# Kernel optimization log

Hardware: AMD Instinct MI355X
Metric: run time of the kernel (lower is better)

Reference implementation:

```python
import jax, jax.numpy as jnp
import numpy as np

BATCH, T, IN, OUT, HID = 8, 4096, 128, 128, 256


def _glorot(key, shape, fan_in, fan_out):
    lim = np.sqrt(6.0 / (fan_in + fan_out))
    return jax.random.uniform(key, shape, jnp.float32, -lim, lim)


def setup_inputs() -> dict:
    key = jax.random.key(0)
    ks = jax.random.split(key, 9)
    # LRU init: r_min=0, r_max=1 => nu = -0.5*log(u), theta = pi/10 * u
    u1 = jax.random.uniform(ks[0], (HID,), jnp.float32, 1e-4, 1.0)
    nu_log = jnp.log(-0.5 * jnp.log(u1))
    theta = (jnp.pi / 10.0) * jax.random.uniform(ks[1], (HID,), jnp.float32, 1e-4, 1.0)
    theta_log = jnp.log(theta)
    return {
        "X": jax.random.normal(ks[2], (BATCH, T, IN), jnp.float32),
        "nu_log": nu_log,
        "theta_log": theta_log,
        "B_re": _glorot(ks[3], (HID, IN), IN, HID),
        "B_im": _glorot(ks[4], (HID, IN), IN, HID),
        "C_re": _glorot(ks[5], (OUT, HID), HID, OUT),
        "C_im": _glorot(ks[6], (OUT, HID), HID, OUT),
        "D": _glorot(ks[7], (OUT, IN), IN, OUT),
    }


def reference(X, nu_log, theta_log, B_re, B_im, C_re, C_im, D):
    # lambda = exp(-exp(nu_log) + 1j*exp(theta_log))  (diagonal complex decay)
    mag = jnp.exp(-jnp.exp(nu_log))            # [H]
    th = jnp.exp(theta_log)                    # [H]
    lam = (mag * jnp.cos(th) + 1j * (mag * jnp.sin(th))).astype(jnp.complex64)
    gamma = jnp.sqrt(1.0 - mag * mag)          # [H]
    Bc = (gamma[:, None] * (B_re + 1j * B_im)).astype(jnp.complex64)  # [H, IN]
    # Input projection: [B, T, H] complex
    BX = jnp.einsum('bti,hi->bth', X.astype(jnp.complex64), Bc)
    lam_b = jnp.broadcast_to(lam, BX.shape)

    def scan_fn(a, b):
        la, xa = a
        lb, xb = b
        return (la * lb, lb * xa + xb)

    _, hiddens = jax.lax.associative_scan(scan_fn, (lam_b, BX), axis=1)
    Cc = (C_re + 1j * C_im).astype(jnp.complex64)
    Y = jnp.real(jnp.einsum('bth,oh->bto', hiddens, Cc)) + jnp.einsum('bti,oi->bto', X, D)
    return Y
```

## Files before the change

kernel.cpp:

```cpp
#include <hip/hip_runtime.h>
#include <hip/hip_bf16.h>

#define TFULL 4096
#define NBATCH 8
#define INDIM 128
#define OUTDIM 128
#define HIDDIM 256
#define LCH 64
#define NCH (TFULL / LCH)

typedef float f32x4 __attribute__((ext_vector_type(4)));
typedef short short8 __attribute__((ext_vector_type(8)));

static __device__ __forceinline__ unsigned short f2bf(float f) {
    unsigned int x = __float_as_uint(f);
    x += 0x7fffu + ((x >> 16) & 1u);
    return (unsigned short)(x >> 16);
}
static __device__ __forceinline__ unsigned int pack2(float a, float b) {
    return ((unsigned int)f2bf(b) << 16) | (unsigned int)f2bf(a);
}
static __device__ __forceinline__ float bflo(unsigned int u) {
    return __uint_as_float(u << 16);
}
static __device__ __forceinline__ float bfhi(unsigned int u) {
    return __uint_as_float(u & 0xffff0000u);
}
static __device__ __forceinline__ void split2(float v, unsigned short& hi, unsigned short& lo) {
    hi = f2bf(v);
    lo = f2bf(v - __uint_as_float((unsigned int)hi << 16));
}

__global__ __launch_bounds__(256) void k_prep(
    const float* __restrict__ nu_log, const float* __restrict__ theta_log,
    const float* __restrict__ C_re, const float* __restrict__ C_im,
    const float* __restrict__ D,
    unsigned short* __restrict__ Wy_hi, unsigned short* __restrict__ Wy_lo,
    float2* __restrict__ lampow)
{
    int f = blockIdx.x * 256 + threadIdx.x;
    if (f < 81920) {
        int q = f;
        int kk = q & 63, o = (q >> 6) & 127, kc = q >> 13;
        int k = 64 * kc + kk;
        float v;
        if (k < 512) {
            int h = k >> 1;
            v = (k & 1) ? -C_im[o * HIDDIM + h] : C_re[o * HIDDIM + h];
        } else {
            v = D[o * INDIM + (k - 512)];
        }
        unsigned short hi, lo; split2(v, hi, lo);
        Wy_hi[q] = hi; Wy_lo[q] = lo;
    } else {
        int l = f - 81920;
        int h = l & 255, tl = l >> 8;
        float nu = expf(nu_log[h]), th = expf(theta_log[h]);
        float kf = (float)(tl + 1);
        float m = expf(-kf * nu);
        lampow[l] = make_float2(m * cosf(kf * th), m * sinf(kf * th));
    }
}

__global__ __launch_bounds__(256) void k_bx_scan(
    const float* __restrict__ X, const float* __restrict__ nu_log,
    const float* __restrict__ theta_log, const float* __restrict__ B_re,
    const float* __restrict__ B_im, unsigned int* __restrict__ hloc,
    float2* __restrict__ EC)
{
    __shared__ float smem[17024];
    float*  XT  = smem;
    float*  Brl = smem + 8704;
    float*  Bil = smem + 12864;
    float2* sb  = (float2*)smem;

    const int tid = threadIdx.x;
    const int blk = blockIdx.x;
    const int b   = blk >> 7;
    const int c   = (blk >> 1) & 63;
    const int h0  = (blk & 1) * 128;
    const int t0  = c * LCH;

    {
        const float* Xb = X + ((size_t)(b * TFULL + t0)) * INDIM;
        int r = tid >> 2;
        int q = tid & 3;
        #pragma unroll
        for (int k = 0; k < 8; ++k) {
            int slot = q + k * 4;
            float4 v = *(const float4*)(Xb + (size_t)r * INDIM + slot * 4);
            float* dst = XT + (slot * 4) * 68 + r;
            dst[0]      = v.x;
            dst[68]     = v.y;
            dst[2 * 68] = v.z;
            dst[3 * 68] = v.w;
        }
    }

    float accre[8][4], accim[8][4];
    #pragma unroll
    for (int r = 0; r < 8; ++r)
        #pragma unroll
        for (int j = 0; j < 4; ++j) { accre[r][j] = 0.f; accim[r][j] = 0.f; }

    const int ty = tid >> 5;
    const int tx = tid & 31;

    for (int kc = 0; kc < 4; ++kc) {
        __syncthreads();
        {
            int hr = tid >> 1;
            int s  = tid & 1;
            int hg = h0 + hr;
            float mag = expf(-expf(nu_log[hg]));
            float gam = sqrtf(fmaxf(0.f, 1.f - mag * mag));
            const float* br = B_re + (size_t)hg * INDIM + kc * 32;
            const float* bi = B_im + (size_t)hg * INDIM + kc * 32;
            #pragma unroll
            for (int q = 0; q < 4; ++q) {
                int col = s * 16 + q * 4;
                float4 vr = *(const float4*)(br + col);
                float4 vi = *(const float4*)(bi + col);
                Brl[(col + 0) * 130 + hr] = vr.x * gam;
                Brl[(col + 1) * 130 + hr] = vr.y * gam;
                Brl[(col + 2) * 130 + hr] = vr.z * gam;
                Brl[(col + 3) * 130 + hr] = vr.w * gam;
                Bil[(col + 0) * 130 + hr] = vi.x * gam;
                Bil[(col + 1) * 130 + hr] = vi.y * gam;
                Bil[(col + 2) * 130 + hr] = vi.z * gam;
                Bil[(col + 3) * 130 + hr] = vi.w * gam;
            }
        }
        __syncthreads();
        for (int kk = 0; kk < 32; ++kk) {
            const float* xrow = XT + (kc * 32 + kk) * 68 + ty * 8;
            float4 xa = *(const float4*)(xrow);
            float4 xb = *(const float4*)(xrow + 4);
            float2 br0 = *(const float2*)(Brl + kk * 130 + 2 * tx);
            float2 br1 = *(const float2*)(Brl + kk * 130 + 64 + 2 * tx);
            float2 bi0 = *(const float2*)(Bil + kk * 130 + 2 * tx);
            float2 bi1 = *(const float2*)(Bil + kk * 130 + 64 + 2 * tx);
            float xs[8]  = {xa.x, xa.y, xa.z, xa.w, xb.x, xb.y, xb.z, xb.w};
            float brs[4] = {br0.x, br0.y, br1.x, br1.y};
            float bis[4] = {bi0.x, bi0.y, bi1.x, bi1.y};
            #pragma unroll
            for (int r = 0; r < 8; ++r)
                #pragma unroll
                for (int j = 0; j < 4; ++j) {
                    accre[r][j] = fmaf(xs[r], brs[j], accre[r][j]);
                    accim[r][j] = fmaf(xs[r], bis[j], accim[r][j]);
                }
        }
    }

    __syncthreads();
    #pragma unroll
    for (int r = 0; r < 8; ++r) {
        int t = ty * 8 + r;
        #pragma unroll
        for (int j = 0; j < 4; ++j) {
            int hl = (j < 2) ? (2 * tx + j) : (64 + 2 * tx + (j - 2));
            sb[t * 130 + hl] = make_float2(accre[r][j], accim[r][j]);
        }
    }
    __syncthreads();

    if (tid < 128) {
        int hl = tid, hg = h0 + hl;
        float nu = expf(nu_log[hg]), th = expf(theta_log[hg]);
        float mag = expf(-nu);
        float lre = mag * cosf(th), lim = mag * sinf(th);
        float sre = 0.f, sim = 0.f;
        unsigned int* hout = hloc + (size_t)(b * TFULL + t0) * HIDDIM + h0 + hl;
        for (int t = 0; t < LCH; ++t) {
            float2 v = sb[t * 130 + hl];
            float nre = fmaf(lre, sre, fmaf(-lim, sim, v.x));
            float nim = fmaf(lre, sim, fmaf(lim, sre, v.y));
            sre = nre; sim = nim;
            hout[(size_t)t * HIDDIM] = pack2(sre, sim);
        }
        EC[((size_t)b * NCH + c) * HIDDIM + h0 + hl] = make_float2(sre, sim);
    }
}

__global__ __launch_bounds__(256) void k_carry(
    const float* __restrict__ nu_log, const float* __restrict__ theta_log,
    float2* __restrict__ EC)
{
    int b = blockIdx.x, h = threadIdx.x;
    float nu = expf(nu_log[h]), th = expf(theta_log[h]);
    float m = expf(-(float)LCH * nu);
    float Lre = m * cosf((float)LCH * th);
    float Lim = m * sinf((float)LCH * th);
    float cre = 0.f, cim = 0.f;
    for (int c = 0; c < NCH; ++c) {
        size_t idx = ((size_t)b * NCH + c) * HIDDIM + h;
        float2 e = EC[idx];
        EC[idx] = make_float2(cre, cim);
        float nre = e.x + Lre * cre - Lim * cim;
        float nim = e.y + Lre * cim + Lim * cre;
        cre = nre; cim = nim;
    }
}

__global__ __launch_bounds__(256) void k_y(
    const float* __restrict__ X, const unsigned int* __restrict__ hloc,
    const float2* __restrict__ EC, const float2* __restrict__ lampow,
    const unsigned short* __restrict__ Wy_hi,
    const unsigned short* __restrict__ Wy_lo, float* __restrict__ Y)
{
    __shared__ unsigned short sm[27648];
    unsigned short* Ah = sm;
    unsigned short* Al = sm + 4608;
    unsigned short* Bh = sm + 9216;
    unsigned short* Bl = sm + 18432;
    __shared__ float2 carryS[256];

    const int tid = threadIdx.x;
    const int b = blockIdx.x >> 6, c = blockIdx.x & 63;
    const size_t rowbase = (size_t)(b * TFULL + c * LCH);

    carryS[tid] = EC[((size_t)b * NCH + c) * HIDDIM + tid];

    f32x4 acc[2][4];
    #pragma unroll
    for (int mi = 0; mi < 2; ++mi)
        #pragma unroll
        for (int nj = 0; nj < 4; ++nj) acc[mi][nj] = (f32x4){0.f, 0.f, 0.f, 0.f};

    const int w = tid >> 6, l = tid & 63;
    const int wm = w >> 1, wn = w & 1;
    const int lr = l & 15, lk = l >> 4;

    for (int kc = 0; kc < 10; ++kc) {
        __syncthreads();
        {
            const uint4* sh = (const uint4*)(Wy_hi + kc * 8192);
            const uint4* sl = (const uint4*)(Wy_lo + kc * 8192);
            #pragma unroll
            for (int j = 0; j < 4; ++j) {
                uint4 vh = sh[tid + j * 256];
                uint4 vl = sl[tid + j * 256];
                int o = (tid >> 3) + 32 * j, kq = 8 * (tid & 7);
                *(uint4*)(Bh + o * 72 + kq) = vh;
                *(uint4*)(Bl + o * 72 + kq) = vl;
            }
        }
        if (kc < 8) {
            #pragma unroll
            for (int s = 0; s < 2; ++s) {
                int f = s * 256 + tid;
                int t = f >> 3, slot = f & 7;
                uint4 u = *(const uint4*)(hloc + (rowbase + t) * HIDDIM + 32 * kc + 4 * slot);
                unsigned int* Arh = (unsigned int*)Ah + t * 36 + 4 * slot;
                unsigned int* Arl = (unsigned int*)Al + t * 36 + 4 * slot;
                const unsigned int* uu = (const unsigned int*)&u;
                #pragma unroll
                for (int e = 0; e < 4; ++e) {
                    int h = 32 * kc + 4 * slot + e;
                    float2 lp = lampow[t * HIDDIM + h];
                    float2 cr = carryS[h];
                    float hre = bflo(uu[e]) + lp.x * cr.x - lp.y * cr.y;
                    float him = bfhi(uu[e]) + lp.x * cr.y + lp.y * cr.x;
                    unsigned short rh, rl, ih, il;
                    split2(hre, rh, rl); split2(him, ih, il);
                    Arh[e] = ((unsigned int)ih << 16) | rh;
                    Arl[e] = ((unsigned int)il << 16) | rl;
                }
            }
        } else {
            int i0 = (kc - 8) * 64;
            #pragma unroll
            for (int s = 0; s < 4; ++s) {
                int f = s * 256 + tid;
                int t = f >> 4, slot = f & 15;
                float4 v = *(const float4*)(X + (rowbase + t) * INDIM + i0 + 4 * slot);
                unsigned short h0,l0,h1,l1,h2,l2,h3,l3;
                split2(v.x,h0,l0); split2(v.y,h1,l1); split2(v.z,h2,l2); split2(v.w,h3,l3);
                unsigned int* Arh = (unsigned int*)Ah + t * 36 + 2 * slot;
                unsigned int* Arl = (unsigned int*)Al + t * 36 + 2 * slot;
                Arh[0] = ((unsigned int)h1 << 16) | h0;
                Arh[1] = ((unsigned int)h3 << 16) | h2;
                Arl[0] = ((unsigned int)l1 << 16) | l0;
                Arl[1] = ((unsigned int)l3 << 16) | l2;
            }
        }
        __syncthreads();
        #pragma unroll
        for (int ks = 0; ks < 2; ++ks) {
            short8 a0h = *(const short8*)(Ah + (32 * wm + lr) * 72 + 32 * ks + 8 * lk);
            short8 a1h = *(const short8*)(Ah + (32 * wm + 16 + lr) * 72 + 32 * ks + 8 * lk);
            short8 a0l = *(const short8*)(Al + (32 * wm + lr) * 72 + 32 * ks + 8 * lk);
            short8 a1l = *(const short8*)(Al + (32 * wm + 16 + lr) * 72 + 32 * ks + 8 * lk);
            #pragma unroll
            for (int nj = 0; nj < 4; ++nj) {
                short8 bh = *(const short8*)(Bh + (64 * wn + 16 * nj + lr) * 72 + 32 * ks + 8 * lk);
                short8 bl = *(const short8*)(Bl + (64 * wn + 16 * nj + lr) * 72 + 32 * ks + 8 * lk);
                acc[0][nj] = __builtin_amdgcn_mfma_f32_16x16x32_bf16(a0h, bh, acc[0][nj], 0, 0, 0);
                acc[0][nj] = __builtin_amdgcn_mfma_f32_16x16x32_bf16(a0h, bl, acc[0][nj], 0, 0, 0);
                acc[0][nj] = __builtin_amdgcn_mfma_f32_16x16x32_bf16(a0l, bh, acc[0][nj], 0, 0, 0);
                acc[1][nj] = __builtin_amdgcn_mfma_f32_16x16x32_bf16(a1h, bh, acc[1][nj], 0, 0, 0);
                acc[1][nj] = __builtin_amdgcn_mfma_f32_16x16x32_bf16(a1h, bl, acc[1][nj], 0, 0, 0);
                acc[1][nj] = __builtin_amdgcn_mfma_f32_16x16x32_bf16(a1l, bh, acc[1][nj], 0, 0, 0);
            }
        }
    }

    float* Yb = Y + rowbase * OUTDIM;
    #pragma unroll
    for (int mi = 0; mi < 2; ++mi)
        #pragma unroll
        for (int nj = 0; nj < 4; ++nj)
            #pragma unroll
            for (int r = 0; r < 4; ++r) {
                int t = 32 * wm + 16 * mi + 4 * lk + r;
                int o = 64 * wn + 16 * nj + lr;
                Yb[(size_t)t * OUTDIM + o] = acc[mi][nj][r];
            }
}

extern "C" void kernel_launch(void* const* d_in, const int* in_sizes, int n_in,
                              void* d_out, int out_size, void* d_ws, size_t ws_size,
                              hipStream_t stream) {
    const float* X         = (const float*)d_in[0];
    const float* nu_log    = (const float*)d_in[1];
    const float* theta_log = (const float*)d_in[2];
    const float* B_re      = (const float*)d_in[3];
    const float* B_im      = (const float*)d_in[4];
    const float* C_re      = (const float*)d_in[5];
    const float* C_im      = (const float*)d_in[6];
    const float* D         = (const float*)d_in[7];
    float* Y = (float*)d_out;

    unsigned int*   hloc   = (unsigned int*)d_ws;
    float2*         EC     = (float2*)((char*)d_ws + (size_t)33554432);
    float2*         lampow = (float2*)((char*)d_ws + (size_t)34603008);
    unsigned short* Wy_hi  = (unsigned short*)((char*)d_ws + (size_t)34996224);
    unsigned short* Wy_lo  = (unsigned short*)((char*)d_ws + (size_t)35160064);

    hipLaunchKernelGGL(k_prep, dim3(384), dim3(256), 0, stream,
                       nu_log, theta_log, C_re, C_im, D, Wy_hi, Wy_lo, lampow);
    hipLaunchKernelGGL(k_bx_scan, dim3(NBATCH * NCH * 2), dim3(256), 0, stream,
                       X, nu_log, theta_log, B_re, B_im, hloc, EC);
    hipLaunchKernelGGL(k_carry, dim3(NBATCH), dim3(256), 0, stream,
                       nu_log, theta_log, EC);
    hipLaunchKernelGGL(k_y, dim3(NBATCH * NCH), dim3(256), 0, stream,
                       X, hloc, EC, lampow, Wy_hi, Wy_lo, Y);
}
```

Before: 174.8 us.

## Move input projection to bf16x3 MFMA and split scan into separate kernel

The FP32 FMA input projection is replaced by a split-bf16 (hi/lo, three-product) MFMA GEMM. Gamma-scaled B weights are now pre-split once in the prep kernel. The per-chunk scan moves into its own kernel that works in place on an fp32 BX buffer. This uses matrix cores for the projection and lets all 256 threads run the scan instead of 128. In exchange, intermediate hidden states are now stored as fp32 complex rather than packed bf16, which doubles that workspace traffic, and there is one more kernel launch.

```diff
diff --git a/kernel.cpp b/kernel.cpp
--- a/kernel.cpp
+++ b/kernel.cpp
@@ -17,15 +17,6 @@
     x += 0x7fffu + ((x >> 16) & 1u);
     return (unsigned short)(x >> 16);
 }
-static __device__ __forceinline__ unsigned int pack2(float a, float b) {
-    return ((unsigned int)f2bf(b) << 16) | (unsigned int)f2bf(a);
-}
-static __device__ __forceinline__ float bflo(unsigned int u) {
-    return __uint_as_float(u << 16);
-}
-static __device__ __forceinline__ float bfhi(unsigned int u) {
-    return __uint_as_float(u & 0xffff0000u);
-}
 static __device__ __forceinline__ void split2(float v, unsigned short& hi, unsigned short& lo) {
     hi = f2bf(v);
     lo = f2bf(v - __uint_as_float((unsigned int)hi << 16));
@@ -33,14 +24,26 @@
 
 __global__ __launch_bounds__(256) void k_prep(
     const float* __restrict__ nu_log, const float* __restrict__ theta_log,
+    const float* __restrict__ B_re, const float* __restrict__ B_im,
     const float* __restrict__ C_re, const float* __restrict__ C_im,
     const float* __restrict__ D,
+    unsigned short* __restrict__ Wbx_hi, unsigned short* __restrict__ Wbx_lo,
     unsigned short* __restrict__ Wy_hi, unsigned short* __restrict__ Wy_lo,
     float2* __restrict__ lampow)
 {
     int f = blockIdx.x * 256 + threadIdx.x;
-    if (f < 81920) {
-        int q = f;
+    if (f < 65536) {
+        int kk = f & 31, n = (f >> 5) & 255, kc = (f >> 13) & 3, half = f >> 15;
+        int g = n >> 6;
+        int h = 128 * half + 64 * (g >> 1) + (n & 63);
+        int i = 32 * kc + kk;
+        float mag = expf(-expf(nu_log[h]));
+        float gam = sqrtf(fmaxf(0.f, 1.f - mag * mag));
+        float v = gam * ((g & 1) ? B_im[h * INDIM + i] : B_re[h * INDIM + i]);
+        unsigned short hi, lo; split2(v, hi, lo);
+        Wbx_hi[f] = hi; Wbx_lo[f] = lo;
+    } else if (f < 147456) {
+        int q = f - 65536;
         int kk = q & 63, o = (q >> 6) & 127, kc = q >> 13;
         int k = 64 * kc + kk;
         float v;
@@ -53,7 +56,7 @@
         unsigned short hi, lo; split2(v, hi, lo);
         Wy_hi[q] = hi; Wy_lo[q] = lo;
     } else {
-        int l = f - 81920;
+        int l = f - 147456;
         int h = l & 255, tl = l >> 8;
         float nu = expf(nu_log[h]), th = expf(theta_log[h]);
         float kf = (float)(tl + 1);
@@ -62,125 +65,118 @@
     }
 }
 
-__global__ __launch_bounds__(256) void k_bx_scan(
-    const float* __restrict__ X, const float* __restrict__ nu_log,
-    const float* __restrict__ theta_log, const float* __restrict__ B_re,
-    const float* __restrict__ B_im, unsigned int* __restrict__ hloc,
-    float2* __restrict__ EC)
-{
-    __shared__ float smem[17024];
-    float*  XT  = smem;
-    float*  Brl = smem + 8704;
-    float*  Bil = smem + 12864;
-    float2* sb  = (float2*)smem;
+__global__ __launch_bounds__(256) void k_bx(
+    const float* __restrict__ X,
+    const unsigned short* __restrict__ Wbx_hi,
+    const unsigned short* __restrict__ Wbx_lo,
+    float2* __restrict__ BX)
+{
+    __shared__ unsigned short sm[25600];
+    unsigned short* Ash = sm;
+    unsigned short* Asl = sm + 2560;
+    unsigned short* Bsh = sm + 5120;
+    unsigned short* Bsl = sm + 15360;
 
     const int tid = threadIdx.x;
     const int blk = blockIdx.x;
-    const int b   = blk >> 7;
-    const int c   = (blk >> 1) & 63;
-    const int h0  = (blk & 1) * 128;
-    const int t0  = c * LCH;
-
-    {
-        const float* Xb = X + ((size_t)(b * TFULL + t0)) * INDIM;
-        int r = tid >> 2;
-        int q = tid & 3;
-        #pragma unroll
-        for (int k = 0; k < 8; ++k) {
-            int slot = q + k * 4;
-            float4 v = *(const float4*)(Xb + (size_t)r * INDIM + slot * 4);
-            float* dst = XT + (slot * 4) * 68 + r;
-            dst[0]      = v.x;
-            dst[68]     = v.y;
-            dst[2 * 68] = v.z;
-            dst[3 * 68] = v.w;
-        }
-    }
-
-    float accre[8][4], accim[8][4];
+    const int b = blk >> 7, c = (blk >> 1) & 63, half = blk & 1;
+    const size_t rowbase = (size_t)(b * TFULL + c * LCH);
+
+    f32x4 acc[2][8];
     #pragma unroll
-    for (int r = 0; r < 8; ++r)
-        #pragma unroll
-        for (int j = 0; j < 4; ++j) { accre[r][j] = 0.f; accim[r][j] = 0.f; }
-
-    const int ty = tid >> 5;
-    const int tx = tid & 31;
+    for (int mi = 0; mi < 2; ++mi)
+        #pragma unroll
+        for (int j = 0; j < 8; ++j) acc[mi][j] = (f32x4){0.f, 0.f, 0.f, 0.f};
+
+    const int w = tid >> 6, l = tid & 63;
+    const int wm = w >> 1, wn = w & 1;
+    const int lr = l & 15, lk = l >> 4;
+    const unsigned short* wch_h = Wbx_hi + half * 32768;
+    const unsigned short* wch_l = Wbx_lo + half * 32768;
 
     for (int kc = 0; kc < 4; ++kc) {
         __syncthreads();
         {
-            int hr = tid >> 1;
-            int s  = tid & 1;
-            int hg = h0 + hr;
-            float mag = expf(-expf(nu_log[hg]));
-            float gam = sqrtf(fmaxf(0.f, 1.f - mag * mag));
-            const float* br = B_re + (size_t)hg * INDIM + kc * 32;
-            const float* bi = B_im + (size_t)hg * INDIM + kc * 32;
-            #pragma unroll
-            for (int q = 0; q < 4; ++q) {
-                int col = s * 16 + q * 4;
-                float4 vr = *(const float4*)(br + col);
-                float4 vi = *(const float4*)(bi + col);
-                Brl[(col + 0) * 130 + hr] = vr.x * gam;
-                Brl[(col + 1) * 130 + hr] = vr.y * gam;
-                Brl[(col + 2) * 130 + hr] = vr.z * gam;
-                Brl[(col + 3) * 130 + hr] = vr.w * gam;
-                Bil[(col + 0) * 130 + hr] = vi.x * gam;
-                Bil[(col + 1) * 130 + hr] = vi.y * gam;
-                Bil[(col + 2) * 130 + hr] = vi.z * gam;
-                Bil[(col + 3) * 130 + hr] = vi.w * gam;
+            const uint4* sh = (const uint4*)(wch_h + kc * 8192);
+            const uint4* sl = (const uint4*)(wch_l + kc * 8192);
+            #pragma unroll
+            for (int j = 0; j < 4; ++j) {
+                uint4 vh = sh[tid + j * 256];
+                uint4 vl = sl[tid + j * 256];
+                int n = (tid >> 2) + 64 * j, kq = 8 * (tid & 3);
+                *(uint4*)(Bsh + n * 40 + kq) = vh;
+                *(uint4*)(Bsl + n * 40 + kq) = vl;
+            }
+        }
+        {
+            int t = tid >> 2, q = tid & 3;
+            const float* Xr = X + (rowbase + t) * INDIM + 32 * kc + 8 * q;
+            float4 v0 = *(const float4*)(Xr);
+            float4 v1 = *(const float4*)(Xr + 4);
+            float xs[8] = {v0.x, v0.y, v0.z, v0.w, v1.x, v1.y, v1.z, v1.w};
+            unsigned int* Ah32 = (unsigned int*)Ash + t * 20 + 4 * q;
+            unsigned int* Al32 = (unsigned int*)Asl + t * 20 + 4 * q;
+            #pragma unroll
+            for (int e = 0; e < 4; ++e) {
+                unsigned short h0, l0, h1, l1;
+                split2(xs[2 * e], h0, l0);
+                split2(xs[2 * e + 1], h1, l1);
+                Ah32[e] = ((unsigned int)h1 << 16) | h0;
+                Al32[e] = ((unsigned int)l1 << 16) | l0;
             }
         }
         __syncthreads();
-        for (int kk = 0; kk < 32; ++kk) {
-            const float* xrow = XT + (kc * 32 + kk) * 68 + ty * 8;
-            float4 xa = *(const float4*)(xrow);
-            float4 xb = *(const float4*)(xrow + 4);
-            float2 br0 = *(const float2*)(Brl + kk * 130 + 2 * tx);
-            float2 br1 = *(const float2*)(Brl + kk * 130 + 64 + 2 * tx);
-            float2 bi0 = *(const float2*)(Bil + kk * 130 + 2 * tx);
-            float2 bi1 = *(const float2*)(Bil + kk * 130 + 64 + 2 * tx);
-            float xs[8]  = {xa.x, xa.y, xa.z, xa.w, xb.x, xb.y, xb.z, xb.w};
-            float brs[4] = {br0.x, br0.y, br1.x, br1.y};
-            float bis[4] = {bi0.x, bi0.y, bi1.x, bi1.y};
-            #pragma unroll
-            for (int r = 0; r < 8; ++r)
-                #pragma unroll
-                for (int j = 0; j < 4; ++j) {
-                    accre[r][j] = fmaf(xs[r], brs[j], accre[r][j]);
-                    accim[r][j] = fmaf(xs[r], bis[j], accim[r][j]);
-                }
-        }
-    }
-
-    __syncthreads();
+        short8 a0h = *(const short8*)(Ash + (32 * wm + lr) * 40 + 8 * lk);
+        short8 a1h = *(const short8*)(Ash + (32 * wm + 16 + lr) * 40 + 8 * lk);
+        short8 a0l = *(const short8*)(Asl + (32 * wm + lr) * 40 + 8 * lk);
+        short8 a1l = *(const short8*)(Asl + (32 * wm + 16 + lr) * 40 + 8 * lk);
+        #pragma unroll
+        for (int j = 0; j < 8; ++j) {
+            short8 bh = *(const short8*)(Bsh + (128 * wn + 16 * j + lr) * 40 + 8 * lk);
+            short8 bl = *(const short8*)(Bsl + (128 * wn + 16 * j + lr) * 40 + 8 * lk);
+            acc[0][j] = __builtin_amdgcn_mfma_f32_16x16x32_bf16(a0h, bh, acc[0][j], 0, 0, 0);
+            acc[0][j] = __builtin_amdgcn_mfma_f32_16x16x32_bf16(a0l, bh, acc[0][j], 0, 0, 0);
+            acc[0][j] = __builtin_amdgcn_mfma_f32_16x16x32_bf16(a0h, bl, acc[0][j], 0, 0, 0);
+            acc[1][j] = __builtin_amdgcn_mfma_f32_16x16x32_bf16(a1h, bh, acc[1][j], 0, 0, 0);
+            acc[1][j] = __builtin_amdgcn_mfma_f32_16x16x32_bf16(a1l, bh, acc[1][j], 0, 0, 0);
+            acc[1][j] = __builtin_amdgcn_mfma_f32_16x16x32_bf16(a1h, bl, acc[1][j], 0, 0, 0);
+        }
+    }
+
     #pragma unroll
-    for (int r = 0; r < 8; ++r) {
-        int t = ty * 8 + r;
-        #pragma unroll
-        for (int j = 0; j < 4; ++j) {
-            int hl = (j < 2) ? (2 * tx + j) : (64 + 2 * tx + (j - 2));
-            sb[t * 130 + hl] = make_float2(accre[r][j], accim[r][j]);
-        }
-    }
-    __syncthreads();
-
-    if (tid < 128) {
-        int hl = tid, hg = h0 + hl;
-        float nu = expf(nu_log[hg]), th = expf(theta_log[hg]);
-        float mag = expf(-nu);
-        float lre = mag * cosf(th), lim = mag * sinf(th);
-        float sre = 0.f, sim = 0.f;
-        unsigned int* hout = hloc + (size_t)(b * TFULL + t0) * HIDDIM + h0 + hl;
-        for (int t = 0; t < LCH; ++t) {
-            float2 v = sb[t * 130 + hl];
-            float nre = fmaf(lre, sre, fmaf(-lim, sim, v.x));
-            float nim = fmaf(lre, sim, fmaf(lim, sre, v.y));
-            sre = nre; sim = nim;
-            hout[(size_t)t * HIDDIM] = pack2(sre, sim);
-        }
-        EC[((size_t)b * NCH + c) * HIDDIM + h0 + hl] = make_float2(sre, sim);
-    }
+    for (int mi = 0; mi < 2; ++mi)
+        #pragma unroll
+        for (int j = 0; j < 4; ++j)
+            #pragma unroll
+            for (int r = 0; r < 4; ++r) {
+                int t = 32 * wm + 16 * mi + 4 * lk + r;
+                int h = 128 * half + 64 * wn + 16 * j + lr;
+                BX[(rowbase + t) * HIDDIM + h] =
+                    make_float2(acc[mi][j][r], acc[mi][j + 4][r]);
+            }
+}
+
+__global__ __launch_bounds__(256) void k_scan(
+    const float* __restrict__ nu_log, const float* __restrict__ theta_log,
+    float2* __restrict__ BX, float2* __restrict__ EC)
+{
+    const int b = blockIdx.x >> 6, c = blockIdx.x & 63;
+    const int h = threadIdx.x;
+    const size_t rowbase = (size_t)(b * TFULL + c * LCH);
+
+    float nu = expf(nu_log[h]), th = expf(theta_log[h]);
+    float mag = expf(-nu);
+    float lre = mag * cosf(th), lim = mag * sinf(th);
+    float sre = 0.f, sim = 0.f;
+    float2* p = BX + rowbase * HIDDIM + h;
+    for (int t = 0; t < LCH; ++t) {
+        float2 v = p[(size_t)t * HIDDIM];
+        float nre = fmaf(lre, sre, fmaf(-lim, sim, v.x));
+        float nim = fmaf(lre, sim, fmaf(lim, sre, v.y));
+        sre = nre; sim = nim;
+        p[(size_t)t * HIDDIM] = make_float2(sre, sim);
+    }
+    EC[((size_t)b * NCH + c) * HIDDIM + h] = make_float2(sre, sim);
 }
 
 __global__ __launch_bounds__(256) void k_carry(
@@ -204,7 +200,7 @@
 }
 
 __global__ __launch_bounds__(256) void k_y(
-    const float* __restrict__ X, const unsigned int* __restrict__ hloc,
+    const float* __restrict__ X, const float2* __restrict__ BXh,
     const float2* __restrict__ EC, const float2* __restrict__ lampow,
     const unsigned short* __restrict__ Wy_hi,
     const unsigned short* __restrict__ Wy_lo, float* __restrict__ Y)
@@ -251,17 +247,19 @@
             for (int s = 0; s < 2; ++s) {
                 int f = s * 256 + tid;
                 int t = f >> 3, slot = f & 7;
-                uint4 u = *(const uint4*)(hloc + (rowbase + t) * HIDDIM + 32 * kc + 4 * slot);
+                const float4* hp =
+                    (const float4*)(BXh + (rowbase + t) * HIDDIM + 32 * kc + 4 * slot);
+                float4 p0 = hp[0], p1 = hp[1];
+                float hv[8] = {p0.x, p0.y, p0.z, p0.w, p1.x, p1.y, p1.z, p1.w};
                 unsigned int* Arh = (unsigned int*)Ah + t * 36 + 4 * slot;
                 unsigned int* Arl = (unsigned int*)Al + t * 36 + 4 * slot;
-                const unsigned int* uu = (const unsigned int*)&u;
                 #pragma unroll
                 for (int e = 0; e < 4; ++e) {
                     int h = 32 * kc + 4 * slot + e;
                     float2 lp = lampow[t * HIDDIM + h];
                     float2 cr = carryS[h];
-                    float hre = bflo(uu[e]) + lp.x * cr.x - lp.y * cr.y;
-                    float him = bfhi(uu[e]) + lp.x * cr.y + lp.y * cr.x;
+                    float hre = hv[2 * e]     + lp.x * cr.x - lp.y * cr.y;
+                    float him = hv[2 * e + 1] + lp.x * cr.y + lp.y * cr.x;
                     unsigned short rh, rl, ih, il;
                     split2(hre, rh, rl); split2(him, ih, il);
                     Arh[e] = ((unsigned int)ih << 16) | rh;
@@ -332,18 +330,23 @@
     const float* D         = (const float*)d_in[7];
     float* Y = (float*)d_out;
 
-    unsigned int*   hloc   = (unsigned int*)d_ws;
-    float2*         EC     = (float2*)((char*)d_ws + (size_t)33554432);
-    float2*         lampow = (float2*)((char*)d_ws + (size_t)34603008);
-    unsigned short* Wy_hi  = (unsigned short*)((char*)d_ws + (size_t)34996224);
-    unsigned short* Wy_lo  = (unsigned short*)((char*)d_ws + (size_t)35160064);
-
-    hipLaunchKernelGGL(k_prep, dim3(384), dim3(256), 0, stream,
-                       nu_log, theta_log, C_re, C_im, D, Wy_hi, Wy_lo, lampow);
-    hipLaunchKernelGGL(k_bx_scan, dim3(NBATCH * NCH * 2), dim3(256), 0, stream,
-                       X, nu_log, theta_log, B_re, B_im, hloc, EC);
+    float2*         BX     = (float2*)d_ws;
+    float2*         EC     = (float2*)((char*)d_ws + (size_t)67108864);
+    float2*         lampow = (float2*)((char*)d_ws + (size_t)68157440);
+    unsigned short* Wbx_hi = (unsigned short*)((char*)d_ws + (size_t)68288512);
+    unsigned short* Wbx_lo = (unsigned short*)((char*)d_ws + (size_t)68419584);
+    unsigned short* Wy_hi  = (unsigned short*)((char*)d_ws + (size_t)68550656);
+    unsigned short* Wy_lo  = (unsigned short*)((char*)d_ws + (size_t)68714496);
+
+    hipLaunchKernelGGL(k_prep, dim3(640), dim3(256), 0, stream,
+                       nu_log, theta_log, B_re, B_im, C_re, C_im, D,
+                       Wbx_hi, Wbx_lo, Wy_hi, Wy_lo, lampow);
+    hipLaunchKernelGGL(k_bx, dim3(NBATCH * NCH * 2), dim3(256), 0, stream,
+                       X, Wbx_hi, Wbx_lo, BX);
+    hipLaunchKernelGGL(k_scan, dim3(NBATCH * NCH), dim3(256), 0, stream,
+                       nu_log, theta_log, BX, EC);
     hipLaunchKernelGGL(k_carry, dim3(NBATCH), dim3(256), 0, stream,
                        nu_log, theta_log, EC);
     hipLaunchKernelGGL(k_y, dim3(NBATCH * NCH), dim3(256), 0, stream,
-                       X, hloc, EC, lampow, Wy_hi, Wy_lo, Y);
-}
+                       X, BX, EC, lampow, Wy_hi, Wy_lo, Y);
+}
```

Result: faster. 154.1 us (-11.8%).
